# Kernel optimization log

Measured on AMD Instinct MI355X. Metric: run time of the kernel, lower is better.

The kernel has to match this reference:

```python
import jax, jax.numpy as jnp
import numpy as np

N_USERS = 200000
N_ITEMS = 100000
EMB_DIM = 64
N_INTER = 2000000


def setup_inputs() -> dict:
    key = jax.random.key(0)
    k_u, k_i, k_ue, k_ie = jax.random.split(key, 4)
    # random bipartite interactions
    u = np.asarray(jax.random.randint(k_u, (N_INTER,), 0, N_USERS), dtype=np.int64)
    i = np.asarray(jax.random.randint(k_i, (N_INTER,), 0, N_ITEMS), dtype=np.int64)
    # symmetric COO edges of the (n_users+n_items) adjacency, as in build_adj
    rows = np.concatenate([u, i + N_USERS])
    cols = np.concatenate([i + N_USERS, u])
    N = N_USERS + N_ITEMS
    deg = np.bincount(rows, minlength=N).astype(np.float32)
    d_inv_sqrt = np.where(deg > 0, deg ** -0.5, 0.0).astype(np.float32)
    vals = d_inv_sqrt[rows] * d_inv_sqrt[cols]  # D^-1/2 A D^-1/2 values
    # xavier_uniform for nn.Embedding weight: bound = sqrt(6/(fan_in+fan_out))
    bu = float(np.sqrt(6.0 / (N_USERS + EMB_DIM)))
    bi = float(np.sqrt(6.0 / (N_ITEMS + EMB_DIM)))
    user_emb = jax.random.uniform(k_ue, (N_USERS, EMB_DIM), jnp.float32, -bu, bu)
    item_emb = jax.random.uniform(k_ie, (N_ITEMS, EMB_DIM), jnp.float32, -bi, bi)
    return {
        "user_emb": user_emb,
        "item_emb": item_emb,
        "vals": jnp.asarray(vals),
        "rows": jnp.asarray(rows, dtype=jnp.int32),
        "cols": jnp.asarray(cols, dtype=jnp.int32),
        "n_layers": 3,
    }


def reference(user_emb, item_emb, vals, rows, cols, n_layers):
    n_users = user_emb.shape[0]
    N = n_users + item_emb.shape[0]
    all_emb = jnp.concatenate([user_emb, item_emb], axis=0)  # [N, D]
    acc = all_emb  # running sum over layers (equiv. to stack+mean)
    for _ in range(n_layers):
        # sparse mm: out[r] += v * emb[c] for each edge (r, c, v)
        msgs = vals[:, None] * all_emb[cols]  # [E, D]
        all_emb = jax.ops.segment_sum(msgs, rows, num_segments=N)
        acc = acc + all_emb
    final = acc / jnp.asarray(n_layers + 1, dtype=acc.dtype)
    return final[:n_users], final[n_users:]
```

## Files before the change

### kernel.cpp

```cpp
#include <hip/hip_runtime.h>
#include <hip/hip_fp16.h>

#define DIM 64
#define RW 8
#define CH 4096
#define BROWS 256
#define BSH 8
#define CBITS 19
#define CMASK ((1u << CBITS) - 1u)
#define SCAN_T 256
#define SCAN_I 16
#define SCAN_CHUNK (SCAN_T * SCAN_I)


__global__ void k_cnt(const int* __restrict__ rows, int* __restrict__ cnt,
                      int nchunks, int NB, long long E) {
    extern __shared__ int hist[];
    for (int b = threadIdx.x; b < NB; b += blockDim.x) hist[b] = 0;
    __syncthreads();
    long long beg = (long long)blockIdx.x * CH;
    long long end = beg + CH; if (end > E) end = E;
    for (long long i = beg + threadIdx.x; i < end; i += blockDim.x)
        atomicAdd(&hist[rows[i] >> BSH], 1);
    __syncthreads();
    for (int b = threadIdx.x; b < NB; b += blockDim.x)
        cnt[(long long)b * nchunks + blockIdx.x] = hist[b];
}

__global__ void k_scanA(const int* __restrict__ in, int* __restrict__ partials, long long L) {
    long long base = (long long)blockIdx.x * SCAN_CHUNK + (long long)threadIdx.x * SCAN_I;
    int tsum = 0;
    for (int k = 0; k < SCAN_I; ++k) { long long i = base + k; if (i < L) tsum += in[i]; }
    __shared__ int s[SCAN_T];
    s[threadIdx.x] = tsum; __syncthreads();
    for (int o = SCAN_T / 2; o > 0; o >>= 1) {
        if (threadIdx.x < o) s[threadIdx.x] += s[threadIdx.x + o];
        __syncthreads();
    }
    if (threadIdx.x == 0) partials[blockIdx.x] = s[0];
}

__global__ void k_scanB(int* partials, int nb) {
    if (threadIdx.x == 0 && blockIdx.x == 0) {
        int run = 0;
        for (int i = 0; i < nb; ++i) { int v = partials[i]; partials[i] = run; run += v; }
    }
}

__global__ void k_scanC(int* __restrict__ data, const int* __restrict__ partials, long long L) {
    const int t = threadIdx.x;
    long long base = (long long)blockIdx.x * SCAN_CHUNK + (long long)t * SCAN_I;
    int local[SCAN_I]; int tsum = 0;
    for (int k = 0; k < SCAN_I; ++k) {
        long long i = base + k;
        int d = (i < L) ? data[i] : 0;
        local[k] = tsum; tsum += d;
    }
    __shared__ int s[SCAN_T];
    s[t] = tsum; __syncthreads();
    for (int o = 1; o < SCAN_T; o <<= 1) {
        int v = (t >= o) ? s[t - o] : 0;
        __syncthreads();
        s[t] += v;
        __syncthreads();
    }
    int toff = partials[blockIdx.x] + (s[t] - tsum);
    for (int k = 0; k < SCAN_I; ++k) {
        long long i = base + k;
        if (i < L) data[i] = toff + local[k];
    }
}

__global__ void k_scatter(const int* __restrict__ rows, const int* __restrict__ cols,
                          const int* __restrict__ off, unsigned* __restrict__ ebuf,
                          int nchunks, int NB, long long E) {
    extern __shared__ int cur[];
    for (int b = threadIdx.x; b < NB; b += blockDim.x)
        cur[b] = off[(long long)b * nchunks + blockIdx.x];
    __syncthreads();
    long long beg = (long long)blockIdx.x * CH;
    long long end = beg + CH; if (end > E) end = E;
    for (long long i = beg + threadIdx.x; i < end; i += blockDim.x) {
        int r = rows[i], c = cols[i];
        int p = atomicAdd(&cur[r >> BSH], 1);
        ebuf[p] = ((unsigned)(r & (BROWS - 1)) << CBITS) | (unsigned)c;
    }
}

__global__ void k_finalize(const unsigned* __restrict__ ebuf, const int* __restrict__ off,
                           int* __restrict__ rp, float* __restrict__ dinv,
                           float* __restrict__ dsq, int* __restrict__ colso,
                           const float4* __restrict__ ue4, const float4* __restrict__ ie4,
                           int2* __restrict__ yh4,
                           int nchunks, int NB, long long N, long long NU, long long E) {
    __shared__ int deg[BROWS];
    __shared__ int cur[BROWS];
    __shared__ int s[BROWS];
    __shared__ float sdinv[BROWS];
    const int b = blockIdx.x, t = threadIdx.x;
    const int row0 = b << BSH;
    const int base = off[(long long)b * nchunks];
    const int bend = (b + 1 < NB) ? off[(long long)(b + 1) * nchunks] : (int)E;
    deg[t] = 0;
    __syncthreads();
    for (int i = base + t; i < bend; i += 256)
        atomicAdd(&deg[ebuf[i] >> CBITS], 1);
    __syncthreads();
    int d = deg[t];
    s[t] = d;
    __syncthreads();
    for (int o = 1; o < 256; o <<= 1) {
        int v = (t >= o) ? s[t - o] : 0;
        __syncthreads();
        s[t] += v;
        __syncthreads();
    }
    int p = base + s[t] - d;
    cur[t] = p;
    float di = d > 0 ? rsqrtf((float)d) : 0.0f;
    sdinv[t] = di;
    int row = row0 + t;
    if (row < (int)N) {
        rp[row] = p;
        dinv[row] = di;
        dsq[row] = sqrtf((float)d);
    }
    if (b == 0 && t == 0) rp[N] = (int)E;
    __syncthreads();
    for (int i = base + t; i < bend; i += 256) {
        unsigned w = ebuf[i];
        int lr = (int)(w >> CBITS);
        int c  = (int)(w & CMASK);
        int pp = atomicAdd(&cur[lr], 1);
        colso[pp] = c;
    }
    for (int i = t; i < BROWS * 16; i += 256) {
        int lr = i >> 4;
        long long row2 = (long long)row0 + lr;
        if (row2 >= N) break;
        long long gi = (row2 << 4) + (i & 15);
        float4 v = (row2 < NU) ? ue4[gi] : ie4[gi - (NU << 4)];
        float dd = sdinv[lr];
        __half2 h01 = __floats2half2_rn(v.x * dd, v.y * dd);
        __half2 h23 = __floats2half2_rn(v.z * dd, v.w * dd);
        int2 w2;
        w2.x = *reinterpret_cast<int*>(&h01);
        w2.y = *reinterpret_cast<int*>(&h23);
        yh4[gi] = w2;
    }
}

template<int FINAL>
__global__ void k_spmm3(const int* __restrict__ rp, const int* __restrict__ colso,
                        const float* __restrict__ dinv, const float* __restrict__ dsq,
                        const __half* __restrict__ src,
                        const __half* __restrict__ y1, const __half* __restrict__ y2,
                        const float* __restrict__ ue, const float* __restrict__ ie,
                        __half* __restrict__ dsth, float* __restrict__ accb,
                        long long N, long long NU, float scale) {
    const int lane = threadIdx.x & 63;
    const int gw = blockIdx.x * (blockDim.x >> 6) + (threadIdx.x >> 6);
    int r0 = gw * RW;
    if (r0 >= (int)N) return;
    int r1 = r0 + RW; if (r1 > (int)N) r1 = (int)N;
    int cur = __builtin_amdgcn_readfirstlane(r0);
    int e      = rp[cur];
    int rowend = rp[cur + 1];
    const int eEnd = rp[r1];
    float sreg = 0.0f;

    #define FLUSH() { \
        long long o = ((long long)cur << 6) + lane; \
        float dr = dinv[cur]; \
        if (!FINAL) { \
            dsth[o] = __float2half(sreg * dr * dr); \
        } else { \
            float e0 = (cur < (int)NU) ? ue[o] : ie[o - (NU << 6)]; \
            float yv = __half2float(y1[o]) + __half2float(y2[o]); \
            accb[o] = (e0 + yv * dsq[cur] + sreg * dr) * scale; \
        } \
        sreg = 0.0f; }

    #define STEP(K, G) \
        while (e + (K) >= rowend) { FLUSH(); ++cur; rowend = rp[cur + 1]; } \
        sreg += (G);

    while (e + 8 <= eEnd) {
        int c0 = colso[e + 0], c1 = colso[e + 1], c2 = colso[e + 2], c3 = colso[e + 3];
        int c4 = colso[e + 4], c5 = colso[e + 5], c6 = colso[e + 6], c7 = colso[e + 7];
        float g0 = __half2float(src[((long long)c0 << 6) + lane]);
        float g1 = __half2float(src[((long long)c1 << 6) + lane]);
        float g2 = __half2float(src[((long long)c2 << 6) + lane]);
        float g3 = __half2float(src[((long long)c3 << 6) + lane]);
        float g4 = __half2float(src[((long long)c4 << 6) + lane]);
        float g5 = __half2float(src[((long long)c5 << 6) + lane]);
        float g6 = __half2float(src[((long long)c6 << 6) + lane]);
        float g7 = __half2float(src[((long long)c7 << 6) + lane]);
        STEP(0, g0) STEP(1, g1) STEP(2, g2) STEP(3, g3)
        STEP(4, g4) STEP(5, g5) STEP(6, g6) STEP(7, g7)
        e += 8;
    }
    for (; e < eEnd; ++e) {
        while (e >= rowend) { FLUSH(); ++cur; rowend = rp[cur + 1]; }
        sreg += __half2float(src[((long long)colso[e] << 6) + lane]);
    }
    while (cur < r1) { FLUSH(); ++cur; }
    #undef STEP
    #undef FLUSH
}


__global__ void lgcn_init(const float4* __restrict__ ue, const float4* __restrict__ ie,
                          float4* __restrict__ cur, float4* __restrict__ acc,
                          long long n_user_v4, long long total_v4) {
    long long idx = (long long)blockIdx.x * blockDim.x + threadIdx.x;
    long long stride = (long long)gridDim.x * blockDim.x;
    for (long long i = idx; i < total_v4; i += stride) {
        float4 v = (i < n_user_v4) ? ue[i] : ie[i - n_user_v4];
        cur[i] = v; acc[i] = v;
    }
}

__global__ void lgcn_spmm(const float* __restrict__ vals, const int* __restrict__ rows,
                          const int* __restrict__ cols, const float* __restrict__ cur,
                          float* __restrict__ next, long long nE) {
    long long tid = (long long)blockIdx.x * blockDim.x + threadIdx.x;
    long long stride = (long long)gridDim.x * blockDim.x;
    long long total = nE << 6;
    for (long long i = tid; i < total; i += stride) {
        long long e = i >> 6;
        int d = (int)(i & 63);
        float m = vals[e] * cur[((long long)cols[e] << 6) + d];
        atomicAdd(&next[((long long)rows[e] << 6) + d], m);
    }
}

__global__ void lgcn_acc_add(float4* __restrict__ acc, const float4* __restrict__ nxt,
                             long long total_v4) {
    long long idx = (long long)blockIdx.x * blockDim.x + threadIdx.x;
    long long stride = (long long)gridDim.x * blockDim.x;
    for (long long i = idx; i < total_v4; i += stride) {
        float4 a = acc[i]; float4 b = nxt[i];
        a.x += b.x; a.y += b.y; a.z += b.z; a.w += b.w;
        acc[i] = a;
    }
}

__global__ void lgcn_acc_add_scale(float4* __restrict__ acc, const float4* __restrict__ nxt,
                                   float s, long long total_v4) {
    long long idx = (long long)blockIdx.x * blockDim.x + threadIdx.x;
    long long stride = (long long)gridDim.x * blockDim.x;
    for (long long i = idx; i < total_v4; i += stride) {
        float4 a = acc[i]; float4 b = nxt[i];
        a.x = (a.x + b.x) * s; a.y = (a.y + b.y) * s;
        a.z = (a.z + b.z) * s; a.w = (a.w + b.w) * s;
        acc[i] = a;
    }
}


extern "C" void kernel_launch(void* const* d_in, const int* in_sizes, int n_in,
                              void* d_out, int out_size, void* d_ws, size_t ws_size,
                              hipStream_t stream) {
    const float* ue   = (const float*)d_in[0];
    const float* ie   = (const float*)d_in[1];
    const float* vals = (const float*)d_in[2];
    const int*   rows = (const int*)d_in[3];
    const int*   cols = (const int*)d_in[4];
    const int n_layers = 3;

    const long long n_users = in_sizes[0] / DIM;
    const long long n_items = in_sizes[1] / DIM;
    const long long E       = in_sizes[2];
    const long long N       = n_users + n_items;
    const long long nElem   = N * DIM;
    const long long nV4     = nElem / 4;
    const long long nUserV4 = (n_users * DIM) / 4;

    float* acc = (float*)d_out;
    const int tb = 256;

    const int nchunks = (int)((E + CH - 1) / CH);
    const int NB      = (int)((N + BROWS - 1) / BROWS);
    const long long L = (long long)NB * nchunks;
    const int nbs     = (int)((L + SCAN_CHUNK - 1) / SCAN_CHUNK);

    size_t need = (size_t)nElem * 2 * 3
                + (size_t)(E + (N + 1) + 2 * N + L + nbs + 64) * 4;

    if (ws_size >= need && N < (1LL << CBITS)) {
        char* p = (char*)d_ws;
        __half* yh0  = (__half*)p;                 p += (size_t)nElem * 2;
        __half* yh1  = (__half*)p;                 p += (size_t)nElem * 2;
        __half* yh2  = (__half*)p;                 p += (size_t)nElem * 2;
        int*   colso = (int*)p;                    p += (size_t)E * 4;
        int*   rp    = (int*)p;                    p += (size_t)(N + 1) * 4;
        float* dinv  = (float*)p;                  p += (size_t)N * 4;
        float* dsq   = (float*)p;                  p += (size_t)N * 4;
        int*   cnt   = (int*)p;                    p += (size_t)L * 4;
        int*   partials = (int*)p;
        unsigned* ebuf = (unsigned*)yh2;

        k_cnt<<<nchunks, tb, NB * 4, stream>>>(rows, cnt, nchunks, NB, E);
        k_scanA<<<nbs, SCAN_T, 0, stream>>>(cnt, partials, L);
        k_scanB<<<1, 64, 0, stream>>>(partials, nbs);
        k_scanC<<<nbs, SCAN_T, 0, stream>>>(cnt, partials, L);
        k_scatter<<<nchunks, tb, NB * 4, stream>>>(rows, cols, cnt, ebuf, nchunks, NB, E);
        k_finalize<<<NB, tb, 0, stream>>>(ebuf, cnt, rp, dinv, dsq, colso,
                                          (const float4*)ue, (const float4*)ie, (int2*)yh0,
                                          nchunks, NB, N, n_users, E);

        const int waves  = (int)((N + RW - 1) / RW);
        const int gspmm  = (waves + 3) / 4;
        k_spmm3<0><<<gspmm, tb, 0, stream>>>(rp, colso, dinv, dsq, yh0,
                                             nullptr, nullptr, nullptr, nullptr,
                                             yh1, nullptr, N, n_users, 0.0f);
        k_spmm3<0><<<gspmm, tb, 0, stream>>>(rp, colso, dinv, dsq, yh1,
                                             nullptr, nullptr, nullptr, nullptr,
                                             yh2, nullptr, N, n_users, 0.0f);
        k_spmm3<1><<<gspmm, tb, 0, stream>>>(rp, colso, dinv, dsq, yh2,
                                             yh1, yh2, ue, ie,
                                             nullptr, acc, N, n_users,
                                             1.0f / (float)(n_layers + 1));
    } else {
        float* cur = (float*)d_ws;
        float* nxt = cur + nElem;
        int gridInit = (int)((nV4 + tb - 1) / tb); if (gridInit > 4096) gridInit = 4096;
        lgcn_init<<<gridInit, tb, 0, stream>>>((const float4*)ue, (const float4*)ie,
                                               (float4*)cur, (float4*)acc, nUserV4, nV4);
        for (int l = 0; l < n_layers; ++l) {
            hipMemsetAsync(nxt, 0, (size_t)nElem * 4, stream);
            lgcn_spmm<<<8192, tb, 0, stream>>>(vals, rows, cols, cur, nxt, E);
            if (l == n_layers - 1) {
                lgcn_acc_add_scale<<<gridInit, tb, 0, stream>>>(
                    (float4*)acc, (const float4*)nxt, 1.0f / (float)(n_layers + 1), nV4);
            } else {
                lgcn_acc_add<<<gridInit, tb, 0, stream>>>((float4*)acc, (const float4*)nxt, nV4);
            }
            float* t = cur; cur = nxt; nxt = t;
        }
    }
}
```

Baseline: 483.4 us.

## Unroll SpMM gather to 16, add nontemporal streaming loads/stores, enlarge count chunks

```diff
diff --git a/kernel.cpp b/kernel.cpp
--- a/kernel.cpp
+++ b/kernel.cpp
@@ -3,7 +3,7 @@
 
 #define DIM 64
 #define RW 8
-#define CH 4096
+#define CH 16384
 #define BROWS 256
 #define BSH 8
 #define CBITS 19
@@ -11,6 +11,24 @@
 #define SCAN_T 256
 #define SCAN_I 16
 #define SCAN_CHUNK (SCAN_T * SCAN_I)
+
+typedef float floatx4 __attribute__((ext_vector_type(4)));
+
+__device__ __forceinline__ float4 nt_load_f4(const float4* p) {
+    floatx4 v = __builtin_nontemporal_load((const floatx4*)p);
+    return make_float4(v.x, v.y, v.z, v.w);
+}
+__device__ __forceinline__ float nt_load_f(const float* p) {
+    return __builtin_nontemporal_load(p);
+}
+__device__ __forceinline__ void nt_store_f(float v, float* p) {
+    __builtin_nontemporal_store(v, p);
+}
+__device__ __forceinline__ float nt_load_h2f(const __half* p) {
+    unsigned short u = __builtin_nontemporal_load((const unsigned short*)p);
+    __half h = *reinterpret_cast<__half*>(&u);
+    return __half2float(h);
+}
 
 
 __global__ void k_cnt(const int* __restrict__ rows, int* __restrict__ cnt,
@@ -139,7 +157,8 @@
         long long row2 = (long long)row0 + lr;
         if (row2 >= N) break;
         long long gi = (row2 << 4) + (i & 15);
-        float4 v = (row2 < NU) ? ue4[gi] : ie4[gi - (NU << 4)];
+        float4 v = (row2 < NU) ? nt_load_f4(ue4 + gi)
+                               : nt_load_f4(ie4 + (gi - (NU << 4)));
         float dd = sdinv[lr];
         __half2 h01 = __floats2half2_rn(v.x * dd, v.y * dd);
         __half2 h23 = __floats2half2_rn(v.z * dd, v.w * dd);
@@ -151,7 +170,7 @@
 }
 
 template<int FINAL>
-__global__ void k_spmm3(const int* __restrict__ rp, const int* __restrict__ colso,
+__global__ void k_spmm4(const int* __restrict__ rp, const int* __restrict__ colso,
                         const float* __restrict__ dinv, const float* __restrict__ dsq,
                         const __half* __restrict__ src,
                         const __half* __restrict__ y1, const __half* __restrict__ y2,
@@ -175,9 +194,10 @@
         if (!FINAL) { \
             dsth[o] = __float2half(sreg * dr * dr); \
         } else { \
-            float e0 = (cur < (int)NU) ? ue[o] : ie[o - (NU << 6)]; \
-            float yv = __half2float(y1[o]) + __half2float(y2[o]); \
-            accb[o] = (e0 + yv * dsq[cur] + sreg * dr) * scale; \
+            float e0 = (cur < (int)NU) ? nt_load_f(ue + o) \
+                                       : nt_load_f(ie + (o - (NU << 6))); \
+            float yv = nt_load_h2f(y1 + o) + __half2float(y2[o]); \
+            nt_store_f((e0 + yv * dsq[cur] + sreg * dr) * scale, accb + o); \
         } \
         sreg = 0.0f; }
 
@@ -185,20 +205,25 @@
         while (e + (K) >= rowend) { FLUSH(); ++cur; rowend = rp[cur + 1]; } \
         sreg += (G);
 
-    while (e + 8 <= eEnd) {
-        int c0 = colso[e + 0], c1 = colso[e + 1], c2 = colso[e + 2], c3 = colso[e + 3];
-        int c4 = colso[e + 4], c5 = colso[e + 5], c6 = colso[e + 6], c7 = colso[e + 7];
-        float g0 = __half2float(src[((long long)c0 << 6) + lane]);
-        float g1 = __half2float(src[((long long)c1 << 6) + lane]);
-        float g2 = __half2float(src[((long long)c2 << 6) + lane]);
-        float g3 = __half2float(src[((long long)c3 << 6) + lane]);
-        float g4 = __half2float(src[((long long)c4 << 6) + lane]);
-        float g5 = __half2float(src[((long long)c5 << 6) + lane]);
-        float g6 = __half2float(src[((long long)c6 << 6) + lane]);
-        float g7 = __half2float(src[((long long)c7 << 6) + lane]);
+    #define LOADC(K) int c##K = colso[e + (K)];
+    #define GATH(K)  float g##K = __half2float(src[((long long)c##K << 6) + lane]);
+
+    while (e + 16 <= eEnd) {
+        LOADC(0) LOADC(1) LOADC(2) LOADC(3) LOADC(4) LOADC(5) LOADC(6) LOADC(7)
+        LOADC(8) LOADC(9) LOADC(10) LOADC(11) LOADC(12) LOADC(13) LOADC(14) LOADC(15)
+        GATH(0) GATH(1) GATH(2) GATH(3) GATH(4) GATH(5) GATH(6) GATH(7)
+        GATH(8) GATH(9) GATH(10) GATH(11) GATH(12) GATH(13) GATH(14) GATH(15)
         STEP(0, g0) STEP(1, g1) STEP(2, g2) STEP(3, g3)
         STEP(4, g4) STEP(5, g5) STEP(6, g6) STEP(7, g7)
-        e += 8;
+        STEP(8, g8) STEP(9, g9) STEP(10, g10) STEP(11, g11)
+        STEP(12, g12) STEP(13, g13) STEP(14, g14) STEP(15, g15)
+        e += 16;
+    }
+    while (e + 4 <= eEnd) {
+        LOADC(0) LOADC(1) LOADC(2) LOADC(3)
+        GATH(0) GATH(1) GATH(2) GATH(3)
+        STEP(0, g0) STEP(1, g1) STEP(2, g2) STEP(3, g3)
+        e += 4;
     }
     for (; e < eEnd; ++e) {
         while (e >= rowend) { FLUSH(); ++cur; rowend = rp[cur + 1]; }
@@ -207,6 +232,8 @@
     while (cur < r1) { FLUSH(); ++cur; }
     #undef STEP
     #undef FLUSH
+    #undef LOADC
+    #undef GATH
 }
 
 
@@ -312,13 +339,13 @@
 
         const int waves  = (int)((N + RW - 1) / RW);
         const int gspmm  = (waves + 3) / 4;
-        k_spmm3<0><<<gspmm, tb, 0, stream>>>(rp, colso, dinv, dsq, yh0,
+        k_spmm4<0><<<gspmm, tb, 0, stream>>>(rp, colso, dinv, dsq, yh0,
                                              nullptr, nullptr, nullptr, nullptr,
                                              yh1, nullptr, N, n_users, 0.0f);
-        k_spmm3<0><<<gspmm, tb, 0, stream>>>(rp, colso, dinv, dsq, yh1,
+        k_spmm4<0><<<gspmm, tb, 0, stream>>>(rp, colso, dinv, dsq, yh1,
                                              nullptr, nullptr, nullptr, nullptr,
                                              yh2, nullptr, N, n_users, 0.0f);
-        k_spmm3<1><<<gspmm, tb, 0, stream>>>(rp, colso, dinv, dsq, yh2,
+        k_spmm4<1><<<gspmm, tb, 0, stream>>>(rp, colso, dinv, dsq, yh2,
                                              yh1, yh2, ue, ie,
                                              nullptr, acc, N, n_users,
                                              1.0f / (float)(n_layers + 1));
```

New measurement: 388.1 us, median of 2. 19.7% less time.
